# Performance work log

Measured on AMD Instinct MI355X. Metric: run time of the kernel, lower is better.

Reference implementation:

```python
import jax, jax.numpy as jnp
import numpy as np

D = 1024      # model_dim
H = 2048      # expert hidden_dim
E = 8         # num routed experts
TOP_K = 2
N_SHARED = 1
B, S = 2, 1024


def setup_inputs() -> dict:
    key = jax.random.key(0)
    ks = jax.random.split(key, 12)
    sc = 0.02
    return {
        "hidden": jax.random.normal(ks[0], (B, S, D), jnp.float32),
        # router Linear(D -> E); stored as [in, out]
        "router_w": jax.random.normal(ks[1], (D, E), jnp.float32) * sc,
        "router_b": jnp.zeros((E,), jnp.float32),
        # shared expert (1): Linear(D->H), Linear(H->D)
        "sw1": jax.random.normal(ks[2], (D, H), jnp.float32) * sc,
        "sb1": jnp.zeros((H,), jnp.float32),
        "sw2": jax.random.normal(ks[3], (H, D), jnp.float32) * sc,
        "sb2": jnp.zeros((D,), jnp.float32),
        # routed experts, stacked over E
        "rw1": jax.random.normal(ks[4], (E, D, H), jnp.float32) * sc,
        "rb1": jnp.zeros((E, H), jnp.float32),
        "rw2": jax.random.normal(ks[5], (E, H, D), jnp.float32) * sc,
        "rb2": jnp.zeros((E, D), jnp.float32),
    }


def reference(hidden, router_w, router_b, sw1, sb1, sw2, sb2, rw1, rb1, rw2, rb2):
    b, s, d = hidden.shape
    T = b * s
    flat = hidden.reshape(T, d)                              # [T, D]

    # --- router ---
    router_logits = flat @ router_w + router_b               # [T, E]
    router_probs = jax.nn.softmax(router_logits, axis=-1)
    topk_probs, topk_idx = jax.lax.top_k(router_probs, TOP_K)  # [T, K]

    # per-(token, expert) mixing weight: sum of top-k probs that hit expert e
    weights = jnp.zeros_like(router_probs).at[
        jnp.arange(T)[:, None], topk_idx
    ].add(topk_probs)                                        # [T, E]

    # --- shared expert(s) (1 expert -> mean == itself) ---
    sh = jax.nn.gelu(flat @ sw1 + sb1, approximate=False)    # [T, H]
    shared_out = (sh @ sw2 + sb2) / N_SHARED                 # [T, D]

    # --- routed experts: dense all-expert eval weighted by routing weights ---
    # (identical math to the gather/FFN/index_add loop: weight is 0 for
    #  tokens not routed to expert e)
    h1 = jax.nn.gelu(jnp.einsum('td,edh->teh', flat, rw1) + rb1[None],
                     approximate=False)                      # [T, E, H]
    expert_out = jnp.einsum('teh,ehd->ted', h1, rw2) + rb2[None]  # [T, E, D]
    mixed = jnp.einsum('ted,te->td', expert_out, weights)    # [T, D]

    return (shared_out + mixed).reshape(b, s, d)
```

## Files before the change

### kernel.cpp

```cpp
#include <hip/hip_runtime.h>
#include <hip/hip_bf16.h>

#define T_TOK 2048
#define DDIM  1024
#define HDIM  2048
#define NEXP  8
#define NSEG  9

typedef unsigned short u16;
typedef __attribute__((ext_vector_type(4))) float f32x4;
typedef __attribute__((ext_vector_type(8))) short bf16x8;
typedef __attribute__((ext_vector_type(4))) unsigned short u16x4;
typedef __attribute__((ext_vector_type(8))) unsigned short u16x8;

__device__ __forceinline__ u16 f2bf(float x) {
  union { float f; unsigned int u; } v; v.f = x;
  unsigned int r = v.u + 0x7fffu + ((v.u >> 16) & 1u);
  return (u16)(r >> 16);
}
__device__ __forceinline__ float gelu_fast(float x) {
  float y = x * (1.595769122f + 0.0713548162f * x * x);
  return x / (1.0f + __expf(-y));
}
__device__ __forceinline__ int swz4(int row) {
  return (row & 3) ^ ((row >> 2) & 3);
}

__device__ __forceinline__ void gload16(const void* g, void* l) {
  __builtin_amdgcn_global_load_lds(
      (const __attribute__((address_space(1))) unsigned int*)g,
      (__attribute__((address_space(3))) unsigned int*)l, 16, 0, 0);
}

__global__ __launch_bounds__(256) void router_kernel(
    const float* __restrict__ x, const float* __restrict__ rw,
    const float* __restrict__ rb, u16* __restrict__ xb,
    float* __restrict__ weights, int* __restrict__ counts,
    int* __restrict__ lists)
{
  int wv = threadIdx.x >> 6, lane = threadIdx.x & 63;
  int t = blockIdx.x * 4 + wv;
  const float* xrow = x + (size_t)t * DDIM;
  float acc[NEXP];
#pragma unroll
  for (int e = 0; e < NEXP; e++) acc[e] = 0.f;
#pragma unroll
  for (int i = 0; i < 4; i++) {
    int d0 = i * 256 + lane * 4;
    f32x4 xv = *(const f32x4*)(xrow + d0);
    u16x4 pk;
#pragma unroll
    for (int j = 0; j < 4; j++) {
      float xs = xv[j];
      pk[j] = f2bf(xs);
      const float* wr = rw + (size_t)(d0 + j) * NEXP;
#pragma unroll
      for (int e = 0; e < NEXP; e++) acc[e] = fmaf(xs, wr[e], acc[e]);
    }
    *(u16x4*)(xb + (size_t)t * DDIM + d0) = pk;
  }
#pragma unroll
  for (int off = 32; off >= 1; off >>= 1)
#pragma unroll
    for (int e = 0; e < NEXP; e++) acc[e] += __shfl_xor(acc[e], off);

  if (lane == 0) {
    float lg[NEXP], mx = -1e30f;
#pragma unroll
    for (int e = 0; e < NEXP; e++) { lg[e] = acc[e] + rb[e]; mx = fmaxf(mx, lg[e]); }
    float p[NEXP], s = 0.f;
#pragma unroll
    for (int e = 0; e < NEXP; e++) { p[e] = expf(lg[e] - mx); s += p[e]; }
    float inv = 1.0f / s;
#pragma unroll
    for (int e = 0; e < NEXP; e++) p[e] *= inv;
    int i1 = 0;
#pragma unroll
    for (int e = 1; e < NEXP; e++) if (p[e] > p[i1]) i1 = e;
    int i2 = (i1 == 0) ? 1 : 0;
#pragma unroll
    for (int e = 0; e < NEXP; e++) if (e != i1 && p[e] > p[i2]) i2 = e;
#pragma unroll
    for (int e = 0; e < NEXP; e++)
      weights[(size_t)t * NEXP + e] = (e == i1) ? p[i1] : (e == i2) ? p[i2] : 0.f;
    int p1 = atomicAdd(counts + i1, 1); lists[i1 * T_TOK + p1] = t;
    int p2 = atomicAdd(counts + i2, 1); lists[i2 * T_TOK + p2] = t;
    lists[NEXP * T_TOK + t] = t;
  }
}

__global__ void seg_kernel(int* counts, int* segoff, int* ytab1, int* nyt1,
                           int* ytab2, int* nyt2) {
  counts[NEXP] = T_TOK;
  int off = 0, n1 = 0, n2 = 0;
  for (int e = 0; e < NSEG; e++) {
    segoff[e] = off;
    int c = counts[e];
    for (int my = 0; my * 128 < c; my++) ytab1[n1++] = e * 256 + my;
    for (int my = 0; my * 256 < c; my++) ytab2[n2++] = e * 256 + my;
    off += c;
  }
  *nyt1 = n1;
  *nyt2 = n2;
}

__global__ __launch_bounds__(256) void gemm1_kernel(
    const u16* __restrict__ Xb, const float* __restrict__ rw1,
    const float* __restrict__ sw1, const float* __restrict__ rb1,
    const float* __restrict__ sb1, const int* __restrict__ counts,
    const int* __restrict__ segoff, const int* __restrict__ lists,
    const int* __restrict__ ytab, const int* __restrict__ nyt,
    u16* __restrict__ H1)
{
  __shared__ u16 Alds[128 * 64];
  __shared__ u16 Blds[128 * 64];

  int tid = threadIdx.x, lane = tid & 63;
  int wv = tid >> 6, wm = wv >> 1, wn = wv & 1;
  int kc = lane >> 4, lr = lane & 15;

  int srow[4]; int achk[4];
#pragma unroll
  for (int r = 0; r < 4; r++) {
    srow[r] = r * 32 + wv * 8 + (lane >> 3);
    achk[r] = ((lane & 7) ^ (srow[r] & 7)) * 8;
  }
  int aoff[2][4], boff[2][4];
#pragma unroll
  for (int ks = 0; ks < 2; ks++)
#pragma unroll
    for (int f = 0; f < 4; f++) {
      int ra = wm * 64 + f * 16 + lr;
      int rb_ = wn * 64 + f * 16 + lr;
      aoff[ks][f] = ra * 64 + (((ks * 4 + kc) ^ (ra & 7)) * 8);
      boff[ks][f] = rb_ * 64 + (((ks * 4 + kc) ^ (rb_ & 7)) * 8);
    }
  int h8 = tid >> 5, bn = (lane & 31) * 4;

  int ntile = nyt[0] * (HDIM / 128);
  for (int t = blockIdx.x; t < ntile; t += gridDim.x) {
    int yt = t >> 4, nx = t & 15;
    int em = ytab[yt];
    int e = em >> 8, m0 = (em & 255) * 128, n0 = nx * 128;
    int cnt = counts[e];
    const float* Wf = (e < NEXP) ? (rw1 + (size_t)e * DDIM * HDIM) : sw1;
    const float* bias = (e < NEXP) ? (rb1 + (size_t)e * HDIM) : sb1;
    const int* list = lists + e * T_TOK;
    int seg = segoff[e];

    size_t asrc[4];
#pragma unroll
    for (int r = 0; r < 4; r++) {
      int tok = list[min(m0 + srow[r], cnt - 1)];
      asrc[r] = (size_t)tok * DDIM + achk[r];
    }
    const float* Wb = Wf + n0 + bn;

    f32x4 acc[4][4];
#pragma unroll
    for (int i = 0; i < 4; i++)
#pragma unroll
      for (int j = 0; j < 4; j++) acc[i][j] = (f32x4){0.f, 0.f, 0.f, 0.f};

    f32x4 vb[8];
    {
      const float* Wk = Wb + (size_t)(h8 * 8) * HDIM;
#pragma unroll
      for (int q = 0; q < 8; q++) vb[q] = *(const f32x4*)(Wk + (size_t)q * HDIM);
    }

    const int NS = DDIM / 64;
    for (int s = 0; s < NS; s++) {
      int kk = s * 64;
#pragma unroll
      for (int r = 0; r < 4; r++)
        gload16(Xb + asrc[r] + kk, Alds + (size_t)(r * 256 + wv * 64 + lane) * 8);
#pragma unroll
      for (int j = 0; j < 4; j++) {
        u16x8 pk;
#pragma unroll
        for (int q = 0; q < 8; q++) pk[q] = f2bf(vb[q][j]);
        int row = bn + j;
        *(u16x8*)(Blds + (size_t)row * 64 + ((h8 ^ (row & 7)) * 8)) = pk;
      }
      __syncthreads();
      if (s + 1 < NS) {
        const float* Wk = Wb + (size_t)((s + 1) * 64 + h8 * 8) * HDIM;
#pragma unroll
        for (int q = 0; q < 8; q++) vb[q] = *(const f32x4*)(Wk + (size_t)q * HDIM);
      }
#pragma unroll
      for (int ks = 0; ks < 2; ks++) {
        bf16x8 af[4], bfr[4];
#pragma unroll
        for (int f = 0; f < 4; f++) {
          af[f]  = *(const bf16x8*)(Alds + aoff[ks][f]);
          bfr[f] = *(const bf16x8*)(Blds + boff[ks][f]);
        }
#pragma unroll
        for (int mf = 0; mf < 4; mf++)
#pragma unroll
          for (int nf = 0; nf < 4; nf++)
            acc[mf][nf] = __builtin_amdgcn_mfma_f32_16x16x32_bf16(af[mf], bfr[nf], acc[mf][nf], 0, 0, 0);
      }
      __syncthreads();
    }

#pragma unroll
    for (int nf = 0; nf < 4; nf++) {
      int col = n0 + wn * 64 + nf * 16 + lr;
      float b = bias[col];
#pragma unroll
      for (int mf = 0; mf < 4; mf++) {
#pragma unroll
        for (int rg = 0; rg < 4; rg++) {
          int mt = wm * 64 + mf * 16 + kc * 4 + rg;
          if (m0 + mt < cnt) {
            float v = acc[mf][nf][rg] + b;
            H1[(size_t)(seg + m0 + mt) * HDIM + col] = f2bf(gelu_fast(v));
          }
        }
      }
    }
  }
}

__global__ __launch_bounds__(512) void gemm2_kernel(
    const u16* __restrict__ H1, const float* __restrict__ rw2,
    const float* __restrict__ sw2, const float* __restrict__ rb2,
    const float* __restrict__ sb2, const float* __restrict__ weights,
    const int* __restrict__ counts, const int* __restrict__ segoff,
    const int* __restrict__ lists, const int* __restrict__ ytab,
    const int* __restrict__ nyt, float* __restrict__ out)
{
  __shared__ u16 Alds[4][256 * 32];
  __shared__ u16 Blds[2][256 * 32];

  int tid = threadIdx.x, lane = tid & 63;
  int wv = tid >> 6, wm = wv >> 2, wn = wv & 3;
  int kc = lane >> 4, lr = lane & 15;

  int srow[2], soff[2];
#pragma unroll
  for (int j = 0; j < 2; j++) {
    int i = j * 512 + tid;
    srow[j] = i >> 2;
    soff[j] = (((i & 3) ^ swz4(i >> 2)) * 8);
  }
  int aoff[8], boff[4];
#pragma unroll
  for (int f = 0; f < 8; f++) {
    int ra = wm * 128 + f * 16 + lr;
    aoff[f] = ra * 32 + ((kc ^ swz4(ra)) * 8);
  }
#pragma unroll
  for (int f = 0; f < 4; f++) {
    int rb_ = wn * 64 + f * 16 + lr;
    boff[f] = rb_ * 32 + ((kc ^ swz4(rb_)) * 8);
  }
  int bw[4];
#pragma unroll
  for (int j = 0; j < 4; j++)
    bw[j] = ((lane << 2) + j) * 32 + (((wv >> 1) ^ j ^ (lane & 3)) << 3) + ((wv & 1) << 2);

  int ntile = nyt[0] * (DDIM / 256) * 2;
  for (int t = blockIdx.x; t < ntile; t += gridDim.x) {
    int kh = t & 1, nx = (t >> 1) & 3, yt = t >> 3;
    int em = ytab[yt];
    int e = em >> 8, m0 = (em & 255) * 256, n0 = nx * 256;
    int cnt = counts[e];
    const float* Wf = (e < NEXP) ? (rw2 + (size_t)e * HDIM * DDIM) : sw2;
    const float* bias = (e < NEXP) ? (rb2 + (size_t)e * DDIM) : sb2;
    const int* list = lists + e * T_TOK;
    int seg = segoff[e];
    int k0 = kh * 1024;

    size_t abase[2];
#pragma unroll
    for (int j = 0; j < 2; j++)
      abase[j] = (size_t)(seg + min(m0 + srow[j], cnt - 1)) * HDIM + k0 + soff[j];
    const float* Wb = Wf + (size_t)k0 * DDIM + n0 + (lane << 2);

    f32x4 acc[8][4];
#pragma unroll
    for (int i = 0; i < 8; i++)
#pragma unroll
      for (int j = 0; j < 4; j++) acc[i][j] = (f32x4){0.f, 0.f, 0.f, 0.f};

    const int NS = 1024 / 32;
    f32x4 vBa, vBb, vBc, vBd;
    {
      const float* Wk = Wb + (size_t)(wv * 4) * DDIM;
      vBa = *(const f32x4*)(Wk);
      vBb = *(const f32x4*)(Wk + DDIM);
      vBc = *(const f32x4*)(Wk + 2 * DDIM);
      vBd = *(const f32x4*)(Wk + 3 * DDIM);
    }
#pragma unroll
    for (int s = 0; s < 2; s++)
#pragma unroll
      for (int j = 0; j < 2; j++) {
        int i = j * 512 + tid;
        gload16(H1 + abase[j] + s * 32, &Alds[s][i * 8]);
      }

    for (int s = 0; s < NS; s++) {
      if (s + 2 < NS) {
        int kk = (s + 2) * 32;
        int nb = (s + 2) & 3;
#pragma unroll
        for (int j = 0; j < 2; j++) {
          int i = j * 512 + tid;
          gload16(H1 + abase[j] + kk, &Alds[nb][i * 8]);
        }
      }
      {
        u16* Bd = &Blds[s & 1][0];
#pragma unroll
        for (int j = 0; j < 4; j++) {
          u16x4 pk;
          pk[0] = f2bf(vBa[j]); pk[1] = f2bf(vBb[j]);
          pk[2] = f2bf(vBc[j]); pk[3] = f2bf(vBd[j]);
          *(u16x4*)(Bd + bw[j]) = pk;
        }
      }
      if (s + 1 < NS) {
        const float* Wk = Wb + (size_t)((s + 1) * 32 + wv * 4) * DDIM;
        vBa = *(const f32x4*)(Wk);
        vBb = *(const f32x4*)(Wk + DDIM);
        vBc = *(const f32x4*)(Wk + 2 * DDIM);
        vBd = *(const f32x4*)(Wk + 3 * DDIM);
      }
      if (s + 2 < NS)      asm volatile("s_waitcnt vmcnt(8)" ::: "memory");
      else if (s + 1 < NS) asm volatile("s_waitcnt vmcnt(6)" ::: "memory");
      else                 asm volatile("s_waitcnt vmcnt(0)" ::: "memory");
      asm volatile("s_waitcnt lgkmcnt(0)" ::: "memory");
      __builtin_amdgcn_s_barrier();
      __builtin_amdgcn_sched_barrier(0);

      const u16* Ac = &Alds[s & 3][0];
      const u16* Bc = &Blds[s & 1][0];
      bf16x8 af[8], bfr[4];
#pragma unroll
      for (int f = 0; f < 8; f++) af[f] = *(const bf16x8*)(Ac + aoff[f]);
#pragma unroll
      for (int f = 0; f < 4; f++) bfr[f] = *(const bf16x8*)(Bc + boff[f]);
      __builtin_amdgcn_s_setprio(1);
#pragma unroll
      for (int mf = 0; mf < 8; mf++)
#pragma unroll
        for (int nf = 0; nf < 4; nf++)
          acc[mf][nf] = __builtin_amdgcn_mfma_f32_16x16x32_bf16(af[mf], bfr[nf], acc[mf][nf], 0, 0, 0);
      __builtin_amdgcn_s_setprio(0);
    }

    float biasv[4];
#pragma unroll
    for (int nf = 0; nf < 4; nf++)
      biasv[nf] = (kh == 0) ? bias[n0 + wn * 64 + nf * 16 + lr] : 0.f;

#pragma unroll
    for (int mf = 0; mf < 8; mf++) {
#pragma unroll
      for (int rg = 0; rg < 4; rg++) {
        int mt = wm * 128 + mf * 16 + kc * 4 + rg;
        int mrow = m0 + mt;
        if (mrow < cnt) {
          int tok = list[mrow];
          float w = (e < NEXP) ? weights[(size_t)tok * NEXP + e] : 1.0f;
          float* orow = out + (size_t)tok * DDIM + n0 + wn * 64 + lr;
#pragma unroll
          for (int nf = 0; nf < 4; nf++)
            atomicAdd(orow + nf * 16, w * (acc[mf][nf][rg] + biasv[nf]));
        }
      }
    }
    __builtin_amdgcn_s_barrier();
    __builtin_amdgcn_sched_barrier(0);
  }
}

extern "C" void kernel_launch(void* const* d_in, const int* in_sizes, int n_in,
                              void* d_out, int out_size, void* d_ws, size_t ws_size,
                              hipStream_t stream) {
  (void)in_sizes; (void)n_in; (void)out_size; (void)ws_size;
  const float* hidden   = (const float*)d_in[0];
  const float* router_w = (const float*)d_in[1];
  const float* router_b = (const float*)d_in[2];
  const float* sw1 = (const float*)d_in[3];
  const float* sb1 = (const float*)d_in[4];
  const float* sw2 = (const float*)d_in[5];
  const float* sb2 = (const float*)d_in[6];
  const float* rw1 = (const float*)d_in[7];
  const float* rb1 = (const float*)d_in[8];
  const float* rw2 = (const float*)d_in[9];
  const float* rb2 = (const float*)d_in[10];
  float* out = (float*)d_out;

  char* ws = (char*)d_ws;
  u16* Xb      = (u16*)(ws + 0);
  u16* H1      = (u16*)(ws + 4194304);
  float* weights = (float*)(ws + 29360128);
  int* counts  = (int*)(ws + 29425664);
  int* segoff  = (int*)(ws + 29425728);
  int* lists   = (int*)(ws + 29425792);
  int* ytab1   = (int*)(ws + 29499520);
  int* nyt1    = (int*)(ws + 29500160);
  int* ytab2   = (int*)(ws + 29500224);
  int* nyt2    = (int*)(ws + 29500864);

  hipMemsetAsync(counts, 0, 64, stream);
  hipMemsetAsync(out, 0, (size_t)T_TOK * DDIM * sizeof(float), stream);

  router_kernel<<<T_TOK / 4, 256, 0, stream>>>(hidden, router_w, router_b, Xb,
                                               weights, counts, lists);
  seg_kernel<<<1, 1, 0, stream>>>(counts, segoff, ytab1, nyt1, ytab2, nyt2);

  gemm1_kernel<<<1024, 256, 0, stream>>>(
      Xb, rw1, sw1, rb1, sb1, counts, segoff, lists, ytab1, nyt1, H1);
  gemm2_kernel<<<256, 512, 0, stream>>>(
      H1, rw2, sw2, rb2, sb2, weights, counts, segoff, lists, ytab2, nyt2, out);
}
```

Before: 233.8 us.

## Enlarge gemm1 M-tile to 256 rows with 512-thread blocks and shared tile table

Changes gemm1 from 128x128 tiles with 256 threads to 256-row M tiles with 512 threads (8 waves), so each fp32 weight tile is loaded and converted to bf16 once per 256 tokens instead of per 128. The A staging buffer doubles, each thread now loads f32x2 weight pairs, and seg_kernel builds one tile table shared by both GEMMs. This halves the weight traffic and conversion per token, at the cost of more padding waste on partially filled expert segments and fewer tiles to spread across CUs.

```diff
diff --git a/kernel.cpp b/kernel.cpp
--- a/kernel.cpp
+++ b/kernel.cpp
@@ -8,6 +8,7 @@
 #define NSEG  9
 
 typedef unsigned short u16;
+typedef __attribute__((ext_vector_type(2))) float f32x2;
 typedef __attribute__((ext_vector_type(4))) float f32x4;
 typedef __attribute__((ext_vector_type(8))) short bf16x8;
 typedef __attribute__((ext_vector_type(4))) unsigned short u16x4;
@@ -89,22 +90,19 @@
   }
 }
 
-__global__ void seg_kernel(int* counts, int* segoff, int* ytab1, int* nyt1,
-                           int* ytab2, int* nyt2) {
+__global__ void seg_kernel(int* counts, int* segoff, int* ytab, int* nyt) {
   counts[NEXP] = T_TOK;
-  int off = 0, n1 = 0, n2 = 0;
+  int off = 0, n = 0;
   for (int e = 0; e < NSEG; e++) {
     segoff[e] = off;
     int c = counts[e];
-    for (int my = 0; my * 128 < c; my++) ytab1[n1++] = e * 256 + my;
-    for (int my = 0; my * 256 < c; my++) ytab2[n2++] = e * 256 + my;
+    for (int my = 0; my * 256 < c; my++) ytab[n++] = e * 256 + my;
     off += c;
   }
-  *nyt1 = n1;
-  *nyt2 = n2;
-}
-
-__global__ __launch_bounds__(256) void gemm1_kernel(
+  *nyt = n;
+}
+
+__global__ __launch_bounds__(512) void gemm1_kernel(
     const u16* __restrict__ Xb, const float* __restrict__ rw1,
     const float* __restrict__ sw1, const float* __restrict__ rb1,
     const float* __restrict__ sb1, const int* __restrict__ counts,
@@ -112,18 +110,19 @@
     const int* __restrict__ ytab, const int* __restrict__ nyt,
     u16* __restrict__ H1)
 {
-  __shared__ u16 Alds[128 * 64];
+  __shared__ u16 Alds[256 * 64];
   __shared__ u16 Blds[128 * 64];
 
   int tid = threadIdx.x, lane = tid & 63;
   int wv = tid >> 6, wm = wv >> 1, wn = wv & 1;
   int kc = lane >> 4, lr = lane & 15;
 
-  int srow[4]; int achk[4];
+  int srow[4], achk[4];
 #pragma unroll
   for (int r = 0; r < 4; r++) {
-    srow[r] = r * 32 + wv * 8 + (lane >> 3);
-    achk[r] = ((lane & 7) ^ (srow[r] & 7)) * 8;
+    int i = r * 512 + tid;
+    srow[r] = i >> 3;
+    achk[r] = ((i & 7) ^ ((i >> 3) & 7)) * 8;
   }
   int aoff[2][4], boff[2][4];
 #pragma unroll
@@ -135,13 +134,13 @@
       aoff[ks][f] = ra * 64 + (((ks * 4 + kc) ^ (ra & 7)) * 8);
       boff[ks][f] = rb_ * 64 + (((ks * 4 + kc) ^ (rb_ & 7)) * 8);
     }
-  int h8 = tid >> 5, bn = (lane & 31) * 4;
+  int bn = lane * 2;
 
   int ntile = nyt[0] * (HDIM / 128);
   for (int t = blockIdx.x; t < ntile; t += gridDim.x) {
     int yt = t >> 4, nx = t & 15;
     int em = ytab[yt];
-    int e = em >> 8, m0 = (em & 255) * 128, n0 = nx * 128;
+    int e = em >> 8, m0 = (em & 255) * 256, n0 = nx * 128;
     int cnt = counts[e];
     const float* Wf = (e < NEXP) ? (rw1 + (size_t)e * DDIM * HDIM) : sw1;
     const float* bias = (e < NEXP) ? (rb1 + (size_t)e * HDIM) : sb1;
@@ -154,7 +153,7 @@
       int tok = list[min(m0 + srow[r], cnt - 1)];
       asrc[r] = (size_t)tok * DDIM + achk[r];
     }
-    const float* Wb = Wf + n0 + bn;
+    const float* Wbp = Wf + n0 + bn;
 
     f32x4 acc[4][4];
 #pragma unroll
@@ -162,11 +161,11 @@
 #pragma unroll
       for (int j = 0; j < 4; j++) acc[i][j] = (f32x4){0.f, 0.f, 0.f, 0.f};
 
-    f32x4 vb[8];
+    f32x2 vb[8];
     {
-      const float* Wk = Wb + (size_t)(h8 * 8) * HDIM;
-#pragma unroll
-      for (int q = 0; q < 8; q++) vb[q] = *(const f32x4*)(Wk + (size_t)q * HDIM);
+      const float* Wk = Wbp + (size_t)(wv * 8) * HDIM;
+#pragma unroll
+      for (int q = 0; q < 8; q++) vb[q] = *(const f32x2*)(Wk + (size_t)q * HDIM);
     }
 
     const int NS = DDIM / 64;
@@ -174,20 +173,20 @@
       int kk = s * 64;
 #pragma unroll
       for (int r = 0; r < 4; r++)
-        gload16(Xb + asrc[r] + kk, Alds + (size_t)(r * 256 + wv * 64 + lane) * 8);
-#pragma unroll
-      for (int j = 0; j < 4; j++) {
+        gload16(Xb + asrc[r] + kk, Alds + (size_t)(r * 512 + tid) * 8);
+#pragma unroll
+      for (int j = 0; j < 2; j++) {
         u16x8 pk;
 #pragma unroll
         for (int q = 0; q < 8; q++) pk[q] = f2bf(vb[q][j]);
         int row = bn + j;
-        *(u16x8*)(Blds + (size_t)row * 64 + ((h8 ^ (row & 7)) * 8)) = pk;
+        *(u16x8*)(Blds + (size_t)row * 64 + ((wv ^ (row & 7)) * 8)) = pk;
       }
       __syncthreads();
       if (s + 1 < NS) {
-        const float* Wk = Wb + (size_t)((s + 1) * 64 + h8 * 8) * HDIM;
-#pragma unroll
-        for (int q = 0; q < 8; q++) vb[q] = *(const f32x4*)(Wk + (size_t)q * HDIM);
+        const float* Wk = Wbp + (size_t)((s + 1) * 64 + wv * 8) * HDIM;
+#pragma unroll
+        for (int q = 0; q < 8; q++) vb[q] = *(const f32x2*)(Wk + (size_t)q * HDIM);
       }
 #pragma unroll
       for (int ks = 0; ks < 2; ks++) {
@@ -404,20 +403,18 @@
   int* counts  = (int*)(ws + 29425664);
   int* segoff  = (int*)(ws + 29425728);
   int* lists   = (int*)(ws + 29425792);
-  int* ytab1   = (int*)(ws + 29499520);
-  int* nyt1    = (int*)(ws + 29500160);
-  int* ytab2   = (int*)(ws + 29500224);
-  int* nyt2    = (int*)(ws + 29500864);
+  int* ytab    = (int*)(ws + 29499520);
+  int* nyt     = (int*)(ws + 29500160);
 
   hipMemsetAsync(counts, 0, 64, stream);
   hipMemsetAsync(out, 0, (size_t)T_TOK * DDIM * sizeof(float), stream);
 
   router_kernel<<<T_TOK / 4, 256, 0, stream>>>(hidden, router_w, router_b, Xb,
                                                weights, counts, lists);
-  seg_kernel<<<1, 1, 0, stream>>>(counts, segoff, ytab1, nyt1, ytab2, nyt2);
-
-  gemm1_kernel<<<1024, 256, 0, stream>>>(
-      Xb, rw1, sw1, rb1, sb1, counts, segoff, lists, ytab1, nyt1, H1);
+  seg_kernel<<<1, 1, 0, stream>>>(counts, segoff, ytab, nyt);
+
+  gemm1_kernel<<<512, 512, 0, stream>>>(
+      Xb, rw1, sw1, rb1, sb1, counts, segoff, lists, ytab, nyt, H1);
   gemm2_kernel<<<256, 512, 0, stream>>>(
-      H1, rw2, sw2, rb2, sb2, weights, counts, segoff, lists, ytab2, nyt2, out);
-}
+      H1, rw2, sw2, rb2, sb2, weights, counts, segoff, lists, ytab, nyt, out);
+}
```

Result: faster. 225.0 us (-3.8%).
